# Kernel optimization log

Measured on AMD Instinct MI355X. Metric: run time of the kernel, lower is better.

Reference implementation:

```python
import jax, jax.numpy as jnp
import numpy as np

KERNEL = 3          # kernel_size = (3, 3)
DEGREE = 3          # spline_order -> Chebyshev polynomial degree
N_CONVS = 8


def setup_inputs() -> dict:
    key = jax.random.key(0)
    k1, k2, k3, k4 = jax.random.split(key, 4)
    x = jax.random.normal(k1, (16, 16, 128, 128), jnp.float32)
    # per-conv learned params of ChebyshevKANLinear(in=9, out=1), stacked over n_convs
    cheby_coeffs = jax.random.normal(k2, (N_CONVS, KERNEL * KERNEL, DEGREE + 1), jnp.float32) * 0.1
    base_weight = jax.random.normal(k3, (N_CONVS, KERNEL * KERNEL), jnp.float32) * (1.0 / 3.0)
    spline_scaler = 1.0 + 0.1 * jax.random.normal(k4, (N_CONVS, KERNEL * KERNEL), jnp.float32)
    return {"x": x, "cheby_coeffs": cheby_coeffs,
            "base_weight": base_weight, "spline_scaler": spline_scaler}


def _kan_conv2d(x, cheby_coeffs, base_weight, spline_scaler):
    # x: (B, C, H, W); each channel unfolded independently (as torch Unfold per-channel),
    # each of N_CONVS KAN kernels applied to every channel -> out channels C*N_CONVS.
    B, C, H, W = x.shape
    patches = jax.lax.conv_general_dilated_patches(
        x, (KERNEL, KERNEL), (1, 1), [(1, 1), (1, 1)])  # (B, C*9, Ho, Wo), channel-major
    Ho, Wo = patches.shape[-2], patches.shape[-1]
    p = patches.reshape(B, C, KERNEL * KERNEL, Ho * Wo)
    p = jnp.moveaxis(p, 2, 3)  # (B, C, P, 9) where P = Ho*Wo patches

    # base (skip) path: SiLU(x) @ base_weight^T
    base = jnp.einsum('bcpi,ji->bcjp', jax.nn.silu(p), base_weight)

    # spline path: Chebyshev basis on tanh-normalized input
    t = jnp.tanh(p)
    Ts = [jnp.ones_like(t), t]
    for _ in range(DEGREE - 1):
        Ts.append(2.0 * t * Ts[-1] - Ts[-2])
    Tb = jnp.stack(Ts, axis=-1)  # (B, C, P, 9, DEGREE+1)
    w = cheby_coeffs * spline_scaler[..., None]  # (n_convs, 9, D+1)
    spline = jnp.einsum('bcpik,jik->bcjp', Tb, w)

    out = (base + spline).reshape(B, C * N_CONVS, Ho, Wo)
    return out


def reference(x, cheby_coeffs, base_weight, spline_scaler):
    return _kan_conv2d(x, cheby_coeffs, base_weight, spline_scaler)
```

## Files before the change

### kernel.cpp

```cpp
#include <hip/hip_runtime.h>

#define BATCH 16
#define CH    16
#define HH    128
#define WW    128
#define NC    8
#define TR    8
#define HR    (TR + 2)
#define FW    (WW + 2)

__global__ __launch_bounds__(256, 4)
void kan_conv_kernel(const float* __restrict__ x,
                     const float* __restrict__ cheby,
                     const float* __restrict__ bwt,
                     const float* __restrict__ scl,
                     float* __restrict__ out)
{
    __shared__ float4 feat[HR][FW];
    __shared__ float4 wgt[9 * NC];
    __shared__ float  bias[NC];

    const int tid  = threadIdx.x;
    const int band = blockIdx.x * TR;
    const int bz   = blockIdx.y;

    if (tid < 9 * NC) {
        int j = tid / 9, i = tid % 9;
        float s = scl[j * 9 + i];
        wgt[i * NC + j] = make_float4(bwt[j * 9 + i],
                                      cheby[(j * 9 + i) * 4 + 1] * s,
                                      cheby[(j * 9 + i) * 4 + 2] * s,
                                      cheby[(j * 9 + i) * 4 + 3] * s);
    } else if (tid >= 128 && tid < 128 + NC) {
        int j = tid - 128;
        float b = 0.f;
        #pragma unroll
        for (int i = 0; i < 9; ++i)
            b += (cheby[(j * 9 + i) * 4 + 0] - cheby[(j * 9 + i) * 4 + 2]) * scl[j * 9 + i];
        bias[j] = b;
    }

    const float* xp = x + (size_t)bz * HH * WW;
    for (int idx = tid; idx < HR * FW; idx += 256) {
        int row = idx / FW;
        int col = idx - row * FW;
        int gh  = band + row - 1;
        int gw  = col - 1;
        float v = 0.f;
        if ((unsigned)gh < (unsigned)HH && (unsigned)gw < (unsigned)WW)
            v = xp[gh * WW + gw];
        float e1 = __expf(v);
        float e2 = e1 * e1;
        float sg = 1.f - __builtin_amdgcn_rcpf(1.f + e1);
        float t  = 1.f - 2.f * __builtin_amdgcn_rcpf(e2 + 1.f);
        float f2 = 2.f * t * t;
        float f3 = 2.f * t * (f2 - 1.f) - t;
        feat[row][col] = make_float4(v * sg, t, f2, f3);
    }
    __syncthreads();

    const int c  = tid & 127;
    const int r0 = tid >> 7;

    float acc[4][NC];
    #pragma unroll
    for (int s = 0; s < 4; ++s)
        #pragma unroll
        for (int j = 0; j < NC; ++j)
            acc[s][j] = bias[j];

    #pragma unroll
    for (int dr = 0; dr < 3; ++dr) {
        #pragma unroll
        for (int dc = 0; dc < 3; ++dc) {
            float4 f[4];
            #pragma unroll
            for (int s = 0; s < 4; ++s)
                f[s] = feat[r0 + 2 * s + dr][c + dc];
            #pragma unroll
            for (int j = 0; j < NC; ++j) {
                float4 w = wgt[(dr * 3 + dc) * NC + j];
                #pragma unroll
                for (int s = 0; s < 4; ++s) {
                    acc[s][j] += w.x * f[s].x;
                    acc[s][j] += w.y * f[s].y;
                    acc[s][j] += w.z * f[s].z;
                    acc[s][j] += w.w * f[s].w;
                }
            }
        }
    }

    float* op = out + (size_t)(bz * NC) * HH * WW + (size_t)(band + r0) * WW + c;
    #pragma unroll
    for (int j = 0; j < NC; ++j)
        #pragma unroll
        for (int s = 0; s < 4; ++s)
            op[(size_t)j * HH * WW + s * 2 * WW] = acc[s][j];
}

extern "C" void kernel_launch(void* const* d_in, const int* in_sizes, int n_in,
                              void* d_out, int out_size, void* d_ws, size_t ws_size,
                              hipStream_t stream) {
    const float* x     = (const float*)d_in[0];
    const float* cheby = (const float*)d_in[1];
    const float* bwt   = (const float*)d_in[2];
    const float* scl   = (const float*)d_in[3];
    float* out = (float*)d_out;

    dim3 grid(HH / TR, BATCH * CH);
    dim3 block(256);
    hipLaunchKernelGGL(kan_conv_kernel, grid, block, 0, stream, x, cheby, bwt, scl, out);
}
```

Before: 168.5 us.

## Process four row bands per block with register-prefetched next-band loads

Each block now handles four consecutive 8-row bands instead of one, reducing grid size by 4x and amortizing weight/bias setup. The global loads for the next band are issued into registers before the current band's compute, so load latency overlaps the FMA work. This costs extra registers for the prefetch buffer, adds two barriers per band, and shrinks the grid (1024 blocks), which may reduce latency hiding across blocks. Halo rows are still reloaded and their features recomputed per band.

```diff
diff --git a/kernel.cpp b/kernel.cpp
--- a/kernel.cpp
+++ b/kernel.cpp
@@ -6,8 +6,11 @@
 #define WW    128
 #define NC    8
 #define TR    8
+#define BPB   4
 #define HR    (TR + 2)
 #define FW    (WW + 2)
+#define NELEM (HR * FW)
+#define NSTG  ((NELEM + 255) / 256)
 
 __global__ __launch_bounds__(256, 4)
 void kan_conv_kernel(const float* __restrict__ x,
@@ -20,9 +23,11 @@
     __shared__ float4 wgt[9 * NC];
     __shared__ float  bias[NC];
 
-    const int tid  = threadIdx.x;
-    const int band = blockIdx.x * TR;
-    const int bz   = blockIdx.y;
+    const int tid   = threadIdx.x;
+    const int bz    = blockIdx.y;
+    const int band0 = blockIdx.x * (TR * BPB);
+
+    const float* xp = x + (size_t)bz * HH * WW;
 
     if (tid < 9 * NC) {
         int j = tid / 9, i = tid % 9;
@@ -40,63 +45,100 @@
         bias[j] = b;
     }
 
-    const float* xp = x + (size_t)bz * HH * WW;
-    for (int idx = tid; idx < HR * FW; idx += 256) {
-        int row = idx / FW;
-        int col = idx - row * FW;
-        int gh  = band + row - 1;
-        int gw  = col - 1;
-        float v = 0.f;
-        if ((unsigned)gh < (unsigned)HH && (unsigned)gw < (unsigned)WW)
-            v = xp[gh * WW + gw];
-        float e1 = __expf(v);
-        float e2 = e1 * e1;
-        float sg = 1.f - __builtin_amdgcn_rcpf(1.f + e1);
-        float t  = 1.f - 2.f * __builtin_amdgcn_rcpf(e2 + 1.f);
-        float f2 = 2.f * t * t;
-        float f3 = 2.f * t * (f2 - 1.f) - t;
-        feat[row][col] = make_float4(v * sg, t, f2, f3);
+    int srow[NSTG], scol[NSTG];
+    #pragma unroll
+    for (int k = 0; k < NSTG; ++k) {
+        int idx = tid + 256 * k;
+        srow[k] = idx / FW;
+        scol[k] = idx - srow[k] * FW;
     }
-    __syncthreads();
 
-    const int c  = tid & 127;
-    const int r0 = tid >> 7;
+    float v[NSTG];
+    #pragma unroll
+    for (int k = 0; k < NSTG; ++k) {
+        int idx = tid + 256 * k;
+        int gh  = band0 + srow[k] - 1;
+        int gw  = scol[k] - 1;
+        float nv = 0.f;
+        if (idx < NELEM && (unsigned)gh < (unsigned)HH && (unsigned)gw < (unsigned)WW)
+            nv = xp[gh * WW + gw];
+        v[k] = nv;
+    }
 
-    float acc[4][NC];
-    #pragma unroll
-    for (int s = 0; s < 4; ++s)
+    for (int bb = 0; bb < BPB; ++bb) {
+        const int band = band0 + bb * TR;
+
         #pragma unroll
-        for (int j = 0; j < NC; ++j)
-            acc[s][j] = bias[j];
+        for (int k = 0; k < NSTG; ++k) {
+            int idx = tid + 256 * k;
+            if (idx < NELEM) {
+                float val = v[k];
+                float e1 = __expf(val);
+                float e2 = e1 * e1;
+                float sg = 1.f - __builtin_amdgcn_rcpf(1.f + e1);
+                float t  = 1.f - 2.f * __builtin_amdgcn_rcpf(e2 + 1.f);
+                float f2 = 2.f * t * t;
+                float f3 = 2.f * t * (f2 - 1.f) - t;
+                feat[srow[k]][scol[k]] = make_float4(val * sg, t, f2, f3);
+            }
+        }
+        __syncthreads();
 
-    #pragma unroll
-    for (int dr = 0; dr < 3; ++dr) {
+        if (bb + 1 < BPB) {
+            const int nb = band + TR;
+            #pragma unroll
+            for (int k = 0; k < NSTG; ++k) {
+                int idx = tid + 256 * k;
+                int gh  = nb + srow[k] - 1;
+                int gw  = scol[k] - 1;
+                float nv = 0.f;
+                if (idx < NELEM && (unsigned)gh < (unsigned)HH && (unsigned)gw < (unsigned)WW)
+                    nv = xp[gh * WW + gw];
+                v[k] = nv;
+            }
+        }
+
+        const int c  = tid & 127;
+        const int r0 = tid >> 7;
+
+        float acc[4][NC];
         #pragma unroll
-        for (int dc = 0; dc < 3; ++dc) {
-            float4 f[4];
+        for (int s = 0; s < 4; ++s)
             #pragma unroll
-            for (int s = 0; s < 4; ++s)
-                f[s] = feat[r0 + 2 * s + dr][c + dc];
+            for (int j = 0; j < NC; ++j)
+                acc[s][j] = bias[j];
+
+        #pragma unroll
+        for (int dr = 0; dr < 3; ++dr) {
             #pragma unroll
-            for (int j = 0; j < NC; ++j) {
-                float4 w = wgt[(dr * 3 + dc) * NC + j];
+            for (int dc = 0; dc < 3; ++dc) {
+                float4 f[4];
                 #pragma unroll
-                for (int s = 0; s < 4; ++s) {
-                    acc[s][j] += w.x * f[s].x;
-                    acc[s][j] += w.y * f[s].y;
-                    acc[s][j] += w.z * f[s].z;
-                    acc[s][j] += w.w * f[s].w;
+                for (int s = 0; s < 4; ++s)
+                    f[s] = feat[r0 + 2 * s + dr][c + dc];
+                #pragma unroll
+                for (int j = 0; j < NC; ++j) {
+                    float4 w = wgt[(dr * 3 + dc) * NC + j];
+                    #pragma unroll
+                    for (int s = 0; s < 4; ++s) {
+                        acc[s][j] += w.x * f[s].x;
+                        acc[s][j] += w.y * f[s].y;
+                        acc[s][j] += w.z * f[s].z;
+                        acc[s][j] += w.w * f[s].w;
+                    }
                 }
             }
         }
+
+        float* op = out + (size_t)(bz * NC) * HH * WW + (size_t)(band + r0) * WW + c;
+        #pragma unroll
+        for (int j = 0; j < NC; ++j)
+            #pragma unroll
+            for (int s = 0; s < 4; ++s)
+                op[(size_t)j * HH * WW + s * 2 * WW] = acc[s][j];
+
+        __syncthreads();
     }
-
-    float* op = out + (size_t)(bz * NC) * HH * WW + (size_t)(band + r0) * WW + c;
-    #pragma unroll
-    for (int j = 0; j < NC; ++j)
-        #pragma unroll
-        for (int s = 0; s < 4; ++s)
-            op[(size_t)j * HH * WW + s * 2 * WW] = acc[s][j];
 }
 
 extern "C" void kernel_launch(void* const* d_in, const int* in_sizes, int n_in,
@@ -108,7 +150,7 @@
     const float* scl   = (const float*)d_in[3];
     float* out = (float*)d_out;
 
-    dim3 grid(HH / TR, BATCH * CH);
+    dim3 grid(HH / (TR * BPB), BATCH * CH);
     dim3 block(256);
     hipLaunchKernelGGL(kan_conv_kernel, grid, block, 0, stream, x, cheby, bwt, scl, out);
 }
```

Measured after the change: 159.3 us. -5.5%, faster.

## Shrink tiles to 4 rows with 128 threads, reuse column features in registers

Applied to the files above, without the earlier changes.

The row band per block is cut from 8 to 4, with 128 threads, so each thread computes all 4 consecutive output rows of one column. Loop order becomes column-offset outer, and the 6 feature rows for that column are held in registers and reused across the three row offsets. This cuts LDS reads per output. Staging now issues all global loads first, then the transcendental feature math, to overlap load latency. In exchange, halo overhead per block is higher (6 rows staged for 4 output rows) and there are twice as many blocks.

```diff
diff --git a/kernel.cpp b/kernel.cpp
--- a/kernel.cpp
+++ b/kernel.cpp
@@ -5,11 +5,14 @@
 #define HH    128
 #define WW    128
 #define NC    8
-#define TR    8
+#define TR    4
 #define HR    (TR + 2)
 #define FW    (WW + 2)
+#define NELEM (HR * FW)
+#define NTHR  128
+#define NSTG  ((NELEM + NTHR - 1) / NTHR)
 
-__global__ __launch_bounds__(256, 4)
+__global__ __launch_bounds__(NTHR, 4)
 void kan_conv_kernel(const float* __restrict__ x,
                      const float* __restrict__ cheby,
                      const float* __restrict__ bwt,
@@ -31,8 +34,8 @@
                                       cheby[(j * 9 + i) * 4 + 1] * s,
                                       cheby[(j * 9 + i) * 4 + 2] * s,
                                       cheby[(j * 9 + i) * 4 + 3] * s);
-    } else if (tid >= 128 && tid < 128 + NC) {
-        int j = tid - 128;
+    } else if (tid < 9 * NC + NC) {
+        int j = tid - 9 * NC;
         float b = 0.f;
         #pragma unroll
         for (int i = 0; i < 9; ++i)
@@ -41,62 +44,74 @@
     }
 
     const float* xp = x + (size_t)bz * HH * WW;
-    for (int idx = tid; idx < HR * FW; idx += 256) {
+    float v[NSTG];
+    #pragma unroll
+    for (int k = 0; k < NSTG; ++k) {
+        int idx = tid + NTHR * k;
         int row = idx / FW;
         int col = idx - row * FW;
         int gh  = band + row - 1;
         int gw  = col - 1;
-        float v = 0.f;
-        if ((unsigned)gh < (unsigned)HH && (unsigned)gw < (unsigned)WW)
-            v = xp[gh * WW + gw];
-        float e1 = __expf(v);
-        float e2 = e1 * e1;
-        float sg = 1.f - __builtin_amdgcn_rcpf(1.f + e1);
-        float t  = 1.f - 2.f * __builtin_amdgcn_rcpf(e2 + 1.f);
-        float f2 = 2.f * t * t;
-        float f3 = 2.f * t * (f2 - 1.f) - t;
-        feat[row][col] = make_float4(v * sg, t, f2, f3);
+        float nv = 0.f;
+        if (idx < NELEM && (unsigned)gh < (unsigned)HH && (unsigned)gw < (unsigned)WW)
+            nv = xp[gh * WW + gw];
+        v[k] = nv;
+    }
+    #pragma unroll
+    for (int k = 0; k < NSTG; ++k) {
+        int idx = tid + NTHR * k;
+        if (idx < NELEM) {
+            int row = idx / FW;
+            int col = idx - row * FW;
+            float val = v[k];
+            float e1 = __expf(val);
+            float e2 = e1 * e1;
+            float sg = 1.f - __builtin_amdgcn_rcpf(1.f + e1);
+            float t  = 1.f - 2.f * __builtin_amdgcn_rcpf(e2 + 1.f);
+            float f2 = 2.f * t * t;
+            float f3 = 2.f * t * (f2 - 1.f) - t;
+            feat[row][col] = make_float4(val * sg, t, f2, f3);
+        }
     }
     __syncthreads();
 
-    const int c  = tid & 127;
-    const int r0 = tid >> 7;
+    const int c = tid;
 
-    float acc[4][NC];
+    float acc[TR][NC];
     #pragma unroll
-    for (int s = 0; s < 4; ++s)
+    for (int s = 0; s < TR; ++s)
         #pragma unroll
         for (int j = 0; j < NC; ++j)
             acc[s][j] = bias[j];
 
     #pragma unroll
-    for (int dr = 0; dr < 3; ++dr) {
+    for (int dc = 0; dc < 3; ++dc) {
+        float4 f[HR];
         #pragma unroll
-        for (int dc = 0; dc < 3; ++dc) {
-            float4 f[4];
-            #pragma unroll
-            for (int s = 0; s < 4; ++s)
-                f[s] = feat[r0 + 2 * s + dr][c + dc];
+        for (int rr = 0; rr < HR; ++rr)
+            f[rr] = feat[rr][c + dc];
+        #pragma unroll
+        for (int dr = 0; dr < 3; ++dr) {
             #pragma unroll
             for (int j = 0; j < NC; ++j) {
                 float4 w = wgt[(dr * 3 + dc) * NC + j];
                 #pragma unroll
-                for (int s = 0; s < 4; ++s) {
-                    acc[s][j] += w.x * f[s].x;
-                    acc[s][j] += w.y * f[s].y;
-                    acc[s][j] += w.z * f[s].z;
-                    acc[s][j] += w.w * f[s].w;
+                for (int s = 0; s < TR; ++s) {
+                    acc[s][j] += w.x * f[s + dr].x;
+                    acc[s][j] += w.y * f[s + dr].y;
+                    acc[s][j] += w.z * f[s + dr].z;
+                    acc[s][j] += w.w * f[s + dr].w;
                 }
             }
         }
     }
 
-    float* op = out + (size_t)(bz * NC) * HH * WW + (size_t)(band + r0) * WW + c;
+    float* op = out + (size_t)(bz * NC) * HH * WW + (size_t)band * WW + c;
     #pragma unroll
     for (int j = 0; j < NC; ++j)
         #pragma unroll
-        for (int s = 0; s < 4; ++s)
-            op[(size_t)j * HH * WW + s * 2 * WW] = acc[s][j];
+        for (int s = 0; s < TR; ++s)
+            op[(size_t)j * HH * WW + (size_t)s * WW] = acc[s][j];
 }
 
 extern "C" void kernel_launch(void* const* d_in, const int* in_sizes, int n_in,
@@ -109,6 +124,6 @@
     float* out = (float*)d_out;
 
     dim3 grid(HH / TR, BATCH * CH);
-    dim3 block(256);
+    dim3 block(NTHR);
     hipLaunchKernelGGL(kan_conv_kernel, grid, block, 0, stream, x, cheby, bwt, scl, out);
 }
```

Result: faster. 164.4 us (-2.4%).
